# Kernel optimization log

Hardware: AMD Instinct MI355X
Metric: run time of the kernel (lower is better)

Reference implementation:

```python
import jax, jax.numpy as jnp
import numpy as np

B, L, V, E, H = 64, 32, 32000, 512, 1024


def setup_inputs() -> dict:
    key = jax.random.key(0)
    ks = jax.random.split(key, 12)
    s = 0.02
    return {
        "x": jax.random.randint(ks[0], (B, 4 * L), 0, V, dtype=jnp.int32),
        "IsTrain": 1,
        "embedding": jax.random.normal(ks[1], (V, E), jnp.float32) * s,
        "W_csm": jax.random.normal(ks[2], (E, H), jnp.float32) * s,
        "Wx1": jax.random.normal(ks[3], (H, H), jnp.float32) * s,
        "Wh1": jax.random.normal(ks[4], (H, H), jnp.float32) * s,
        "Wx2": jax.random.normal(ks[5], (H, H), jnp.float32) * s,
        "Wh2": jax.random.normal(ks[6], (H, H), jnp.float32) * s,
        "U": jax.random.normal(ks[7], (L, H, H), jnp.float32) * s,
        "Ww": jax.random.normal(ks[8], (V, H), jnp.float32) * s,
        "Wc": jax.random.normal(ks[9], (H, H), jnp.float32) * s,
        "Wfc": jax.random.normal(ks[10], (H, V), jnp.float32) * s,
    }


def _forward(x, embedding, W_csm, Wx1, Wh1, Wx2, Wh2, U, Ww, Wc, Wfc):
    # x: [B, 4L] int token ids (train mode: 4 sentences)
    emb = embedding[x]                                   # [B, 4L, E]

    # CSM: sentence -> vector [B, H] (mean-pool + projection + tanh)
    segs = emb[:, : 3 * L].reshape(x.shape[0], 3, L, E)  # first 3 sentences
    sent = jnp.tanh(jnp.einsum("bse,eh->bsh", segs.mean(axis=2), W_csm))  # [B,3,H]

    # RCM: 2-layer tanh RNN over sentence vectors; hidden after t sentences
    # equals RCM run on the length-t prefix (prefix property of an RNN).
    def step(carry, s_t):
        h1, h2 = carry
        h1 = jnp.tanh(s_t @ Wx1 + h1 @ Wh1)
        h2 = jnp.tanh(h1 @ Wx2 + h2 @ Wh2)
        return (h1, h2), h2

    h0 = jnp.zeros((x.shape[0], H), emb.dtype)
    _, hs = jax.lax.scan(step, (h0, h0), sent.transpose(1, 0, 2))  # [3,B,H]

    # Per-position context vectors: context_k = tanh(h_k @ U_m) for m in [0,L)
    contexts = jnp.tanh(jnp.einsum("sbh,mhk->sbmk", hs, U))        # [3,B,L,H]

    # RGM at step i (i>=1 within each section): prev hidden is always re-zeroed
    # in the original loop, so cur = tanh(onehot(w) @ Ww + ctx @ Wc); the one-hot
    # matmul is expressed as a gather (identical math).
    # Section k, local step i in [1,L): word index = x[:, (k+1)*L + i - 1]
    idx = jnp.stack([x[:, (k + 1) * L : (k + 2) * L - 1] for k in range(3)])  # [3,B,L-1]
    cur = jnp.tanh(Ww[idx] + jnp.einsum("sblh,hk->sblk", contexts[:, :, 1:], Wc))
    y_sec = jnp.einsum("sblh,hv->sblv", cur, Wfc)                  # [3,B,L-1,V]

    # Step 0 of each section: one-hot of the first target word (constant wrt params)
    firsts = x[:, jnp.array([L, 2 * L, 3 * L])].T                   # [3,B]
    first_oh = jax.nn.one_hot(firsts, V, dtype=y_sec.dtype)         # [3,B,V]

    y = jnp.concatenate([first_oh[:, :, None, :], y_sec], axis=2)   # [3,B,L,V]
    return y.transpose(1, 0, 2, 3).reshape(x.shape[0], 3 * L, V)


def reference(x, IsTrain, embedding, W_csm, Wx1, Wh1, Wx2, Wh2, U, Ww, Wc, Wfc):
    # IsTrain must be truthy: this reference implements the training branch.
    return _forward(x, embedding, W_csm, Wx1, Wh1, Wx2, Wh2, U, Ww, Wc, Wfc)
```

## Files before the change

kernel.cpp:

```cpp
#include <hip/hip_runtime.h>
#include <math.h>

typedef __bf16 bf16x8 __attribute__((ext_vector_type(8)));
typedef float f32x4 __attribute__((ext_vector_type(4)));
typedef unsigned short u16;
typedef u16 u16x8 __attribute__((ext_vector_type(8)));

#define DI __device__ __forceinline__

DI u16 f2bf(float f) {
  union { float f; unsigned u; } v; v.f = f;
  unsigned r = v.u + 0x7FFFu + ((v.u >> 16) & 1u);
  return (u16)(r >> 16);
}

DI void gload_lds16(const u16* g, u16* l) {
  __builtin_amdgcn_global_load_lds(
      (const __attribute__((address_space(1))) unsigned int*)g,
      (__attribute__((address_space(3))) unsigned int*)l, 16, 0, 0);
}

DI void grid_bar(int* ctr, int nblk) {
  __syncthreads();
  if (threadIdx.x == 0) {
    __threadfence();
    atomicAdd(ctr, 1);
    while (atomicAdd(ctr, 0) < nblk) { __builtin_amdgcn_s_sleep(8); }
    __threadfence();
  }
  __syncthreads();
}

__global__ __launch_bounds__(256) void meanpool_k(const int* __restrict__ x,
    const float* __restrict__ emb, u16* __restrict__ sentM) {
  int bs = blockIdx.x; int s = bs >> 6, b = bs & 63;
  int t = threadIdx.x;
  float a0 = 0.f, a1 = 0.f;
  for (int lt = 0; lt < 32; ++lt) {
    int tok = x[b * 128 + s * 32 + lt];
    const float* e = emb + (long)tok * 512;
    a0 += e[t]; a1 += e[t + 256];
  }
  sentM[(long)bs * 512 + t] = f2bf(a0 * (1.f / 32.f));
  sentM[(long)bs * 512 + t + 256] = f2bf(a1 * (1.f / 32.f));
}

DI void transpose64_body(const float* __restrict__ in, u16* __restrict__ out,
                         int C, int ostride) {
  __shared__ float tile[32 * 65];
  int c0 = blockIdx.x * 32, r0 = blockIdx.y * 64;
  int t = threadIdx.x;
  int cc = t & 31, rr0 = t >> 5;
#pragma unroll
  for (int i = 0; i < 8; ++i) {
    int rr = rr0 + 8 * i;
    tile[cc * 65 + (rr ^ ((cc & 7) << 3))] = in[(long)(r0 + rr) * C + c0 + cc];
  }
  __syncthreads();
  int cj = t >> 3, rj = t & 7;
  u16x8 v;
#pragma unroll
  for (int k = 0; k < 8; ++k)
    v[k] = f2bf(tile[cj * 65 + ((rj * 8 + k) ^ ((cj & 7) << 3))]);
  *(u16x8*)(out + (long)(c0 + cj) * ostride + r0 + rj * 8) = v;
}

__global__ __launch_bounds__(256) void transpose64(
    const float* __restrict__ in, u16* __restrict__ out, int R, int C,
    int ostride) {
  in += (long)blockIdx.z * (long)R * C;
  out += (long)blockIdx.z * (long)C * ostride;
  transpose64_body(in, out, C, ostride);
}

struct TJob { const float* in; u16* out; int R; int ostride; };
struct TJobs { TJob j[6]; };
__global__ __launch_bounds__(256) void transpose64_multi(TJobs jobs) {
  TJob jb = jobs.j[blockIdx.z];
  if ((int)(blockIdx.y * 64) >= jb.R) return;
  transpose64_body(jb.in, jb.out, 1024, jb.ostride);
}

DI void small_body(u16 (*As)[2048], u16 (*Bs)[4096],
                   const u16* A0, const u16* A1, const u16* Bt, u16* outp,
                   int M, int K, int kSplit, int Astride, int Bstride,
                   int mt, int ntb) {
  const int t = threadIdx.x;
  const int w = t >> 6, l = t & 63, lr = l & 15, lg = l >> 4;
  int ar = mt * 64 + (t & 63); if (ar >= M) ar = M - 1;
  const u16* pB = Bt + (long)(ntb * 128 + (t & 127)) * Bstride + (t >> 7) * 8;
  const int ntk = K >> 5;

  auto STG = [&](int buf, int kt) {
    int k0 = kt << 5;
    const u16* srcA = (k0 < kSplit)
        ? A0 + (long)ar * Astride + k0 + w * 8
        : A1 + (long)ar * 1024 + (k0 - kSplit) + w * 8;
    gload_lds16(srcA, &As[buf][w * 512]);
    gload_lds16(pB + k0, &Bs[buf][w * 512]);
    gload_lds16(pB + k0 + 16, &Bs[buf][2048 + w * 512]);
  };
  STG(0, 0);
  if (ntk > 1) STG(1, 1);

  f32x4 acc[4][2] = {};
  for (int kt = 0; kt < ntk; ++kt) {
    int cb = kt % 3;
    if (kt + 2 < ntk) {
      STG((kt + 2) % 3, kt + 2);
      asm volatile("s_waitcnt vmcnt(6)" ::: "memory");
    } else if (kt + 1 < ntk) {
      asm volatile("s_waitcnt vmcnt(3)" ::: "memory");
    } else {
      asm volatile("s_waitcnt vmcnt(0)" ::: "memory");
    }
    __builtin_amdgcn_s_barrier();
    __builtin_amdgcn_sched_barrier(0);
    bf16x8 a[4], b[2];
#pragma unroll
    for (int mf = 0; mf < 4; ++mf)
      a[mf] = *(const bf16x8*)(&As[cb][(lg * 64 + mf * 16 + lr) * 8]);
#pragma unroll
    for (int nf = 0; nf < 2; ++nf)
      b[nf] = *(const bf16x8*)(&Bs[cb][(lg * 128 + w * 32 + nf * 16 + lr) * 8]);
#pragma unroll
    for (int mf = 0; mf < 4; ++mf)
#pragma unroll
      for (int nf = 0; nf < 2; ++nf)
        acc[mf][nf] = __builtin_amdgcn_mfma_f32_16x16x32_bf16(a[mf], b[nf], acc[mf][nf], 0, 0, 0);
    __builtin_amdgcn_s_barrier();
    __builtin_amdgcn_sched_barrier(0);
  }
#pragma unroll
  for (int mf = 0; mf < 4; ++mf)
#pragma unroll
    for (int j = 0; j < 4; ++j) {
      int r = mt * 64 + mf * 16 + lg * 4 + j;
      if (r < M) {
        u16* o = outp + (long)r * 1024 + ntb * 128 + w * 32;
#pragma unroll
        for (int nf = 0; nf < 2; ++nf)
          o[nf * 16 + lr] = f2bf(tanhf(acc[mf][nf][j]));
      }
    }
}

__global__ __launch_bounds__(256) void rnn_chain(
    const u16* __restrict__ sentM, u16* __restrict__ sentH,
    u16* __restrict__ h1a, u16* __restrict__ h1b, u16* __restrict__ hsb,
    const u16* __restrict__ WcsmT, const u16* __restrict__ WxhT1,
    const u16* __restrict__ WxhT2, int* __restrict__ ctr) {
  __shared__ __align__(16) u16 As[3][2048];
  __shared__ __align__(16) u16 Bs[3][4096];
  int b = blockIdx.x;
  small_body(As, Bs, sentM, sentM, WcsmT, sentH, 192, 512, 512, 512, 512,
             b >> 3, b & 7);
  grid_bar(ctr + 0, 24);
  if (b < 8) small_body(As, Bs, sentH, h1a, WxhT1, h1a,
                        64, 1024, 1024, 1024, 2048, 0, b);
  grid_bar(ctr + 1, 24);
  if (b < 8) small_body(As, Bs, h1a, h1a, WxhT2, hsb,
                        64, 1024, 1024, 1024, 2048, 0, b);
  grid_bar(ctr + 2, 24);
  if (b < 8) small_body(As, Bs, sentH + 65536, h1a, WxhT1, h1b,
                        64, 2048, 1024, 1024, 2048, 0, b);
  grid_bar(ctr + 3, 24);
  if (b < 8) small_body(As, Bs, h1b, hsb, WxhT2, hsb + 65536,
                        64, 2048, 1024, 1024, 2048, 0, b);
  grid_bar(ctr + 4, 24);
  if (b < 8) small_body(As, Bs, sentH + 131072, h1b, WxhT1, h1a,
                        64, 2048, 1024, 1024, 2048, 0, b);
  grid_bar(ctr + 5, 24);
  if (b < 8) small_body(As, Bs, h1a, hsb + 65536, WxhT2, hsb + 131072,
                        64, 2048, 1024, 1024, 2048, 0, b);
}

template <int MODE>
__global__ __launch_bounds__(256) void gemm_bf16(
    const u16* __restrict__ A, const u16* __restrict__ Bt,
    const float* __restrict__ Ww, const int* __restrict__ xtok,
    void* __restrict__ outp, int M) {
  int mt = blockIdx.x, nt = blockIdx.y, mz = blockIdx.z;
  if constexpr (MODE == 0) Bt += (long)mz << 20;

  __shared__ __align__(16) u16 As[128 * 32];
  __shared__ __align__(16) u16 Bs[128 * 32];

  const int t = threadIdx.x;
  const int w = t >> 6, l = t & 63;
  const int lr = l & 15, lg = l >> 4;
  const int wr = w >> 1, wc = w & 1;

  int ar0 = mt * 128 + (t >> 2);
  int ar1 = ar0 + 64;
  if (ar0 >= M) ar0 = 0;
  if (ar1 >= M) ar1 = 0;
  long arow0, arow1;
  if constexpr (MODE == 1) {
    arow0 = (long)(ar0 / 31) * 32 + (ar0 % 31) + 1;
    arow1 = (long)(ar1 / 31) * 32 + (ar1 % 31) + 1;
  } else {
    arow0 = ar0; arow1 = ar1;
  }

  const u16* ga0 = A + arow0 * 1024 + (t & 3) * 8;
  const u16* ga1 = A + arow1 * 1024 + (t & 3) * 8;
  const u16* gb0 = Bt + ((long)nt * 128 + (t >> 2)) * 1024 + (t & 3) * 8;
  const u16* gb1 = gb0 + 64 * 1024;

  u16* dA0 = As + w * 512; u16* dA1 = As + 2048 + w * 512;
  u16* dB0 = Bs + w * 512; u16* dB1 = Bs + 2048 + w * 512;

  f32x4 acc[4][4] = {};

  for (int kt = 0; kt < 32; ++kt) {
    __syncthreads();
    gload_lds16(ga0, dA0); gload_lds16(ga1, dA1);
    gload_lds16(gb0, dB0); gload_lds16(gb1, dB1);
    ga0 += 32; ga1 += 32; gb0 += 32; gb1 += 32;
    __syncthreads();
    bf16x8 a[4], b[4];
#pragma unroll
    for (int m = 0; m < 4; ++m)
      a[m] = *(const bf16x8*)&As[(wr * 64 + m * 16 + lr) * 32 + lg * 8];
#pragma unroll
    for (int n = 0; n < 4; ++n)
      b[n] = *(const bf16x8*)&Bs[(wc * 64 + n * 16 + lr) * 32 + lg * 8];
#pragma unroll
    for (int m = 0; m < 4; ++m)
#pragma unroll
      for (int n = 0; n < 4; ++n)
        acc[m][n] = __builtin_amdgcn_mfma_f32_16x16x32_bf16(a[m], b[n], acc[m][n], 0, 0, 0);
  }

#pragma unroll
  for (int m = 0; m < 4; ++m) {
#pragma unroll
    for (int j = 0; j < 4; ++j) {
      int r = mt * 128 + wr * 64 + m * 16 + lg * 4 + j;
      if (r >= M) continue;
      if constexpr (MODE == 0) {
        u16* oc = (u16*)outp;
#pragma unroll
        for (int n = 0; n < 4; ++n) {
          int col = nt * 128 + wc * 64 + n * 16 + lr;
          oc[((long)r * 32 + mz) * 1024 + col] = f2bf(tanhf(acc[m][n][j]));
        }
      } else {
        int sb = r / 31, l1 = r % 31;
        int s = sb >> 6, b = sb & 63;
        int widx = xtok[b * 128 + (s + 1) * 32 + l1];
        const float* wwr = Ww + (long)widx * 1024;
        u16* oc = (u16*)outp;
#pragma unroll
        for (int n = 0; n < 4; ++n) {
          int col = nt * 128 + wc * 64 + n * 16 + lr;
          oc[(long)r * 1024 + col] = f2bf(tanhf(acc[m][n][j] + wwr[col]));
        }
      }
    }
  }
}

#define NOSTAGE ((void)0)
#define VM4 asm volatile("s_waitcnt vmcnt(4)" ::: "memory")
#define VM0 asm volatile("s_waitcnt vmcnt(0)" ::: "memory")

#define STAGE_A(H, KT) do {                                                \
    const u16* _s = ((H) ? pA1 : pA0) + (KT) * 64;                         \
    u16* _d = lds + ((KT) & 1) * 16384 + (H) * 8192 + w * 512;             \
    gload_lds16(_s, _d); gload_lds16(_s + 32, _d + 4096);                  \
  } while (0)
#define STAGE_B(H, KT) do {                                                \
    const u16* _s = ((H) ? pB1 : pB0) + (KT) * 64;                         \
    u16* _d = lds + 32768 + ((KT) & 1) * 16384 + (H) * 8192 + w * 512;     \
    gload_lds16(_s, _d); gload_lds16(_s + 32, _d + 4096);                  \
  } while (0)

#define PHASE(ABASE, MH, NH, RA, RB, STAGESTMT, WAITSTMT) do {             \
    if (RA) {                                                              \
      _Pragma("unroll") for (int ks = 0; ks < 2; ++ks)                     \
      _Pragma("unroll") for (int mf = 0; mf < 4; ++mf)                     \
        a[mf][ks] = *(const bf16x8*)(lds + (ABASE) + (MH) * 8192 + laneA + \
                                     ks * 4096 + mf * 128);                \
    }                                                                      \
    if (RB) {                                                              \
      _Pragma("unroll") for (int ks = 0; ks < 2; ++ks)                     \
      _Pragma("unroll") for (int nf = 0; nf < 2; ++nf)                     \
        b[NH][nf][ks] = *(const bf16x8*)(lds + 32768 + (ABASE) +           \
                                         (NH) * 8192 + laneB +             \
                                         ks * 4096 + nf * 128);            \
    }                                                                      \
    STAGESTMT;                                                             \
    __builtin_amdgcn_s_barrier();                                          \
    asm volatile("s_waitcnt lgkmcnt(0)" ::: "memory");                     \
    __builtin_amdgcn_sched_barrier(0);                                     \
    __builtin_amdgcn_s_setprio(1);                                         \
    _Pragma("unroll") for (int ks = 0; ks < 2; ++ks)                       \
    _Pragma("unroll") for (int mf = 0; mf < 4; ++mf)                       \
    _Pragma("unroll") for (int nf = 0; nf < 2; ++nf)                       \
      acc[(MH) * 4 + mf][(NH) * 2 + nf] =                                  \
          __builtin_amdgcn_mfma_f32_16x16x32_bf16(                         \
              a[mf][ks], b[NH][nf][ks],                                    \
              acc[(MH) * 4 + mf][(NH) * 2 + nf], 0, 0, 0);                 \
    __builtin_amdgcn_s_setprio(0);                                         \
    WAITSTMT;                                                              \
    __builtin_amdgcn_s_barrier();                                          \
  } while (0)

__global__ __launch_bounds__(512, 2) void gemm_big(
    const u16* __restrict__ A, const u16* __restrict__ Bt,
    const int* __restrict__ x, float* __restrict__ out) {
  __shared__ __align__(16) u16 lds[65536];

  const int t = threadIdx.x;
  const int w = t >> 6, l = t & 63;
  const int lr = l & 15, lg = l >> 4;
  const int wm = w >> 2, wn = w & 3;
  const int laneA = (lg * 128 + wm * 64 + lr) * 8;
  const int laneB = (lg * 128 + wn * 32 + lr) * 8;

  int xcd = blockIdx.x & 7, slot = blockIdx.x >> 3;

  for (int tl = slot; tl < 375; tl += 32) {
    int nt = tl / 3;
    int mt = xcd * 3 + tl % 3;

    int arow0 = mt * 256 + (t & 127);
    int arow1 = arow0 + 128;
    int ar0c = arow0 > 5951 ? 5951 : arow0;
    int ar1c = arow1 > 5951 ? 5951 : arow1;
    const u16* pA0 = A + (long)ar0c * 1024 + (t >> 7) * 8;
    const u16* pA1 = A + (long)ar1c * 1024 + (t >> 7) * 8;
    const u16* pB0 = Bt + ((long)nt * 256 + (t & 127)) * 1024 + (t >> 7) * 8;
    const u16* pB1 = pB0 + 128 * 1024;

    f32x4 acc[8][4] = {};
    bf16x8 a[4][2], b[2][2][2];

    STAGE_A(0, 0); STAGE_B(0, 0); STAGE_B(1, 0); STAGE_A(1, 0);
    STAGE_A(0, 1); STAGE_B(0, 1);
    VM4;
    __builtin_amdgcn_s_barrier();

    for (int g = 0; g < 14; g += 2) {
      PHASE(0,     0, 0, 1, 1, STAGE_B(1, g + 1), NOSTAGE);
      PHASE(0,     0, 1, 0, 1, STAGE_A(1, g + 1), NOSTAGE);
      PHASE(0,     1, 0, 1, 0, STAGE_A(0, g + 2), NOSTAGE);
      PHASE(0,     1, 1, 0, 0, STAGE_B(0, g + 2), VM4);
      PHASE(16384, 0, 0, 1, 1, STAGE_B(1, g + 2), NOSTAGE);
      PHASE(16384, 0, 1, 0, 1, STAGE_A(1, g + 2), NOSTAGE);
      PHASE(16384, 1, 0, 1, 0, STAGE_A(0, g + 3), NOSTAGE);
      PHASE(16384, 1, 1, 0, 0, STAGE_B(0, g + 3), VM4);
    }
    PHASE(0,     0, 0, 1, 1, STAGE_B(1, 15), NOSTAGE);
    PHASE(0,     0, 1, 0, 1, STAGE_A(1, 15), NOSTAGE);
    PHASE(0,     1, 0, 1, 0, NOSTAGE, NOSTAGE);
    PHASE(0,     1, 1, 0, 0, NOSTAGE, VM0);
    PHASE(16384, 0, 0, 1, 1, NOSTAGE, NOSTAGE);
    PHASE(16384, 0, 1, 0, 1, NOSTAGE, NOSTAGE);
    PHASE(16384, 1, 0, 1, 0, NOSTAGE, NOSTAGE);
    PHASE(16384, 1, 1, 0, 0, NOSTAGE, NOSTAGE);

    float* T = (float*)lds + w * 2112;
#pragma unroll
    for (int mh = 0; mh < 2; ++mh)
#pragma unroll
      for (int nh = 0; nh < 2; ++nh) {
#pragma unroll
        for (int mf = 0; mf < 4; ++mf)
#pragma unroll
          for (int j = 0; j < 4; ++j)
#pragma unroll
            for (int nf = 0; nf < 2; ++nf)
              T[(mf * 16 + lg * 4 + j) * 33 + nf * 16 + lr] =
                  acc[mh * 4 + mf][nh * 2 + nf][j];
#pragma unroll
        for (int i = 0; i < 8; ++i) {
          int row = (l >> 3) + 8 * i;
          int c4 = (l & 7) * 4;
          f32x4 v;
          v[0] = T[row * 33 + c4];     v[1] = T[row * 33 + c4 + 1];
          v[2] = T[row * 33 + c4 + 2]; v[3] = T[row * 33 + c4 + 3];
          int r = mt * 256 + mh * 128 + wm * 64 + row;
          int colb = nt * 256 + nh * 128 + wn * 32 + c4;
          float* o;
          if (r < 5952) {
            int s = r / 1984, rem = r % 1984;
            int bb = rem / 31, l1 = rem % 31;
            o = out + ((long)bb * 96 + s * 32 + l1 + 1) * 32000 + colb;
          } else {
            int i2 = r - 5952;
            int s = i2 >> 6, bb = i2 & 63;
            int tok = x[bb * 128 + (s + 1) * 32];
            v[0] = (colb == tok);     v[1] = (colb + 1 == tok);
            v[2] = (colb + 2 == tok); v[3] = (colb + 3 == tok);
            o = out + ((long)bb * 96 + s * 32) * 32000 + colb;
          }
          __builtin_nontemporal_store(v, (f32x4*)o);
        }
      }
    __builtin_amdgcn_s_barrier();
  }
}

extern "C" void kernel_launch(void* const* d_in, const int* in_sizes, int n_in,
                              void* d_out, int out_size, void* d_ws, size_t ws_size,
                              hipStream_t stream) {
  const int*   x    = (const int*)d_in[0];
  const float* emb  = (const float*)d_in[2];
  const float* Wcsm = (const float*)d_in[3];
  const float* Wx1  = (const float*)d_in[4];
  const float* Wh1  = (const float*)d_in[5];
  const float* Wx2  = (const float*)d_in[6];
  const float* Wh2  = (const float*)d_in[7];
  const float* U    = (const float*)d_in[8];
  const float* Ww   = (const float*)d_in[9];
  const float* Wc   = (const float*)d_in[10];
  const float* Wfc  = (const float*)d_in[11];
  float* out = (float*)d_out;

  char* ws = (char*)d_ws;
  u16* sentM = (u16*)(ws + 0);
  u16* sentH = (u16*)(ws + 196608);
  u16* h1a   = (u16*)(ws + 589824);
  u16* h1b   = (u16*)(ws + 720896);
  u16* hsb   = (u16*)(ws + 851968);
  u16* ctx   = (u16*)(ws + 1245184);
  u16* WcsmT = (u16*)(ws + 1245184);
  u16* WxhT1 = (u16*)(ws + 2293760);
  u16* WxhT2 = (u16*)(ws + 6488064);
  u16* cur   = (u16*)(ws + 13828096);
  u16* WcT   = (u16*)(ws + 26017792);
  u16* BIG   = (u16*)(ws + 28114944);
  int* ctr   = (int*)(ws + 28114944 + 67108864 - 64);

  TJobs jobs;
  jobs.j[0] = {Wx1,  WxhT1,        1024, 2048};
  jobs.j[1] = {Wh1,  WxhT1 + 1024, 1024, 2048};
  jobs.j[2] = {Wx2,  WxhT2,        1024, 2048};
  jobs.j[3] = {Wh2,  WxhT2 + 1024, 1024, 2048};
  jobs.j[4] = {Wc,   WcT,          1024, 1024};
  jobs.j[5] = {Wcsm, WcsmT,         512,  512};
  transpose64_multi<<<dim3(32, 16, 6), 256, 0, stream>>>(jobs);

  meanpool_k<<<192, 256, 0, stream>>>(x, emb, sentM);
  hipMemsetAsync((void*)ctr, 0, 64, stream);
  rnn_chain<<<24, 256, 0, stream>>>(sentM, sentH, h1a, h1b, hsb,
                                    WcsmT, WxhT1, WxhT2, ctr);

  transpose64<<<dim3(32, 16, 32), 256, 0, stream>>>(U, BIG, 1024, 1024, 1024);
  gemm_bf16<0><<<dim3(2, 8, 32), 256, 0, stream>>>(hsb, BIG, nullptr, nullptr, (void*)ctx, 192);

  gemm_bf16<1><<<dim3(47, 8, 1), 256, 0, stream>>>(ctx, WcT, Ww, x, (void*)cur, 5952);

  transpose64<<<dim3(1000, 16, 1), 256, 0, stream>>>(Wfc, BIG, 1024, 32000, 1024);
  gemm_big<<<256, 512, 0, stream>>>(cur, BIG, x, out);
}
```

Baseline: 911.4 us.

## Switch final vocab projection GEMM from bf16 to fp8 MFMA with scaling

Converts the activations (cur) and the transposed Wfc weights to fp8 e4m3 with a 16x prescale each and runs the big output GEMM using fp8 MFMA. The accumulator is rescaled by 1/256 at the end. This halves the operand bytes moved and staged through LDS, and it uses the higher-rate fp8 matrix instructions. The LDS layout, load addressing and wait counts are adjusted to match. The cost is a large loss of precision in the dominant GEMM, which may exceed the output tolerance.

```diff
diff --git a/kernel.cpp b/kernel.cpp
--- a/kernel.cpp
+++ b/kernel.cpp
@@ -4,7 +4,9 @@
 typedef __bf16 bf16x8 __attribute__((ext_vector_type(8)));
 typedef float f32x4 __attribute__((ext_vector_type(4)));
 typedef unsigned short u16;
+typedef unsigned char u8;
 typedef u16 u16x8 __attribute__((ext_vector_type(8)));
+typedef u8 u8x8 __attribute__((ext_vector_type(8)));
 
 #define DI __device__ __forceinline__
 
@@ -14,7 +16,19 @@
   return (u16)(r >> 16);
 }
 
-DI void gload_lds16(const u16* g, u16* l) {
+DI u8 f2fp8(float f) {
+  union { float f; unsigned u; } v; v.f = f;
+  unsigned s = (v.u >> 24) & 0x80u;
+  unsigned au = v.u & 0x7FFFFFFFu;
+  unsigned r = au + 0x7FFFFu + ((au >> 20) & 1u);
+  int e = (int)(r >> 23) - 120;
+  unsigned m = (r >> 20) & 7u;
+  if (e <= 0) return (u8)s;
+  if (e > 15 || (e == 15 && m == 7)) return (u8)(s | 0x7E);
+  return (u8)(s | ((unsigned)e << 3) | m);
+}
+
+DI void gload_lds16(const void* g, void* l) {
   __builtin_amdgcn_global_load_lds(
       (const __attribute__((address_space(1))) unsigned int*)g,
       (__attribute__((address_space(3))) unsigned int*)l, 16, 0, 0);
@@ -79,6 +93,26 @@
   TJob jb = jobs.j[blockIdx.z];
   if ((int)(blockIdx.y * 64) >= jb.R) return;
   transpose64_body(jb.in, jb.out, 1024, jb.ostride);
+}
+
+__global__ __launch_bounds__(256) void transpose64_f8(
+    const float* __restrict__ in, u8* __restrict__ out, int C, int ostride) {
+  __shared__ float tile[32 * 65];
+  int c0 = blockIdx.x * 32, r0 = blockIdx.y * 64;
+  int t = threadIdx.x;
+  int cc = t & 31, rr0 = t >> 5;
+#pragma unroll
+  for (int i = 0; i < 8; ++i) {
+    int rr = rr0 + 8 * i;
+    tile[cc * 65 + (rr ^ ((cc & 7) << 3))] = in[(long)(r0 + rr) * C + c0 + cc];
+  }
+  __syncthreads();
+  int cj = t >> 3, rj = t & 7;
+  u8x8 v;
+#pragma unroll
+  for (int k = 0; k < 8; ++k)
+    v[k] = f2fp8(16.f * tile[cj * 65 + ((rj * 8 + k) ^ ((cj & 7) << 3))]);
+  *(u8x8*)(out + (long)(c0 + cj) * ostride + r0 + rj * 8) = v;
 }
 
 DI void small_body(u16 (*As)[2048], u16 (*Bs)[4096],
@@ -251,11 +285,11 @@
         int s = sb >> 6, b = sb & 63;
         int widx = xtok[b * 128 + (s + 1) * 32 + l1];
         const float* wwr = Ww + (long)widx * 1024;
-        u16* oc = (u16*)outp;
+        u8* oc = (u8*)outp;
 #pragma unroll
         for (int n = 0; n < 4; ++n) {
           int col = nt * 128 + wc * 64 + n * 16 + lr;
-          oc[(long)r * 1024 + col] = f2bf(tanhf(acc[m][n][j] + wwr[col]));
+          oc[(long)r * 1024 + col] = f2fp8(16.f * tanhf(acc[m][n][j] + wwr[col]));
         }
       }
     }
@@ -263,33 +297,29 @@
 }
 
 #define NOSTAGE ((void)0)
-#define VM4 asm volatile("s_waitcnt vmcnt(4)" ::: "memory")
+#define VM2 asm volatile("s_waitcnt vmcnt(2)" ::: "memory")
 #define VM0 asm volatile("s_waitcnt vmcnt(0)" ::: "memory")
 
-#define STAGE_A(H, KT) do {                                                \
-    const u16* _s = ((H) ? pA1 : pA0) + (KT) * 64;                         \
-    u16* _d = lds + ((KT) & 1) * 16384 + (H) * 8192 + w * 512;             \
-    gload_lds16(_s, _d); gload_lds16(_s + 32, _d + 4096);                  \
-  } while (0)
-#define STAGE_B(H, KT) do {                                                \
-    const u16* _s = ((H) ? pB1 : pB0) + (KT) * 64;                         \
-    u16* _d = lds + 32768 + ((KT) & 1) * 16384 + (H) * 8192 + w * 512;     \
-    gload_lds16(_s, _d); gload_lds16(_s + 32, _d + 4096);                  \
-  } while (0)
+#define STAGE_A(H, KT) \
+  gload_lds16(((H) ? pA1 : pA0) + (KT) * 64, \
+              ldsb + ((KT) & 1) * 16384 + (H) * 8192 + w * 1024)
+#define STAGE_B(H, KT) \
+  gload_lds16(((H) ? pB1 : pB0) + (KT) * 64, \
+              ldsb + 32768 + ((KT) & 1) * 16384 + (H) * 8192 + w * 1024)
 
 #define PHASE(ABASE, MH, NH, RA, RB, STAGESTMT, WAITSTMT) do {             \
     if (RA) {                                                              \
       _Pragma("unroll") for (int ks = 0; ks < 2; ++ks)                     \
       _Pragma("unroll") for (int mf = 0; mf < 4; ++mf)                     \
-        a[mf][ks] = *(const bf16x8*)(lds + (ABASE) + (MH) * 8192 + laneA + \
-                                     ks * 4096 + mf * 128);                \
+        a[mf][ks] = *(const long*)(ldsb + (ABASE) + (MH) * 8192 + laneA +  \
+                                   ks * 4096 + mf * 256);                  \
     }                                                                      \
     if (RB) {                                                              \
       _Pragma("unroll") for (int ks = 0; ks < 2; ++ks)                     \
       _Pragma("unroll") for (int nf = 0; nf < 2; ++nf)                     \
-        b[NH][nf][ks] = *(const bf16x8*)(lds + 32768 + (ABASE) +           \
-                                         (NH) * 8192 + laneB +             \
-                                         ks * 4096 + nf * 128);            \
+        b[NH][nf][ks] = *(const long*)(ldsb + 32768 + (ABASE) +            \
+                                       (NH) * 8192 + laneB +               \
+                                       ks * 4096 + nf * 256);              \
     }                                                                      \
     STAGESTMT;                                                             \
     __builtin_amdgcn_s_barrier();                                          \
@@ -300,7 +330,7 @@
     _Pragma("unroll") for (int mf = 0; mf < 4; ++mf)                       \
     _Pragma("unroll") for (int nf = 0; nf < 2; ++nf)                       \
       acc[(MH) * 4 + mf][(NH) * 2 + nf] =                                  \
-          __builtin_amdgcn_mfma_f32_16x16x32_bf16(                         \
+          __builtin_amdgcn_mfma_f32_16x16x32_fp8_fp8(                      \
               a[mf][ks], b[NH][nf][ks],                                    \
               acc[(MH) * 4 + mf][(NH) * 2 + nf], 0, 0, 0);                 \
     __builtin_amdgcn_s_setprio(0);                                         \
@@ -309,16 +339,17 @@
   } while (0)
 
 __global__ __launch_bounds__(512, 2) void gemm_big(
-    const u16* __restrict__ A, const u16* __restrict__ Bt,
+    const u8* __restrict__ A, const u8* __restrict__ Bt,
     const int* __restrict__ x, float* __restrict__ out) {
   __shared__ __align__(16) u16 lds[65536];
+  u8* ldsb = (u8*)lds;
 
   const int t = threadIdx.x;
   const int w = t >> 6, l = t & 63;
   const int lr = l & 15, lg = l >> 4;
   const int wm = w >> 2, wn = w & 3;
-  const int laneA = (lg * 128 + wm * 64 + lr) * 8;
-  const int laneB = (lg * 128 + wn * 32 + lr) * 8;
+  const int laneA = (wm * 64 + lr) * 16 + (lg >> 1) * 2048 + (lg & 1) * 8;
+  const int laneB = (wn * 32 + lr) * 16 + (lg >> 1) * 2048 + (lg & 1) * 8;
 
   int xcd = blockIdx.x & 7, slot = blockIdx.x >> 3;
 
@@ -330,28 +361,28 @@
     int arow1 = arow0 + 128;
     int ar0c = arow0 > 5951 ? 5951 : arow0;
     int ar1c = arow1 > 5951 ? 5951 : arow1;
-    const u16* pA0 = A + (long)ar0c * 1024 + (t >> 7) * 8;
-    const u16* pA1 = A + (long)ar1c * 1024 + (t >> 7) * 8;
-    const u16* pB0 = Bt + ((long)nt * 256 + (t & 127)) * 1024 + (t >> 7) * 8;
-    const u16* pB1 = pB0 + 128 * 1024;
+    const u8* pA0 = A + (long)ar0c * 1024 + (t >> 7) * 16;
+    const u8* pA1 = A + (long)ar1c * 1024 + (t >> 7) * 16;
+    const u8* pB0 = Bt + ((long)nt * 256 + (t & 127)) * 1024 + (t >> 7) * 16;
+    const u8* pB1 = pB0 + 128 * 1024;
 
     f32x4 acc[8][4] = {};
-    bf16x8 a[4][2], b[2][2][2];
+    long a[4][2], b[2][2][2];
 
     STAGE_A(0, 0); STAGE_B(0, 0); STAGE_B(1, 0); STAGE_A(1, 0);
     STAGE_A(0, 1); STAGE_B(0, 1);
-    VM4;
+    VM2;
     __builtin_amdgcn_s_barrier();
 
     for (int g = 0; g < 14; g += 2) {
       PHASE(0,     0, 0, 1, 1, STAGE_B(1, g + 1), NOSTAGE);
       PHASE(0,     0, 1, 0, 1, STAGE_A(1, g + 1), NOSTAGE);
       PHASE(0,     1, 0, 1, 0, STAGE_A(0, g + 2), NOSTAGE);
-      PHASE(0,     1, 1, 0, 0, STAGE_B(0, g + 2), VM4);
+      PHASE(0,     1, 1, 0, 0, STAGE_B(0, g + 2), VM2);
       PHASE(16384, 0, 0, 1, 1, STAGE_B(1, g + 2), NOSTAGE);
       PHASE(16384, 0, 1, 0, 1, STAGE_A(1, g + 2), NOSTAGE);
       PHASE(16384, 1, 0, 1, 0, STAGE_A(0, g + 3), NOSTAGE);
-      PHASE(16384, 1, 1, 0, 0, STAGE_B(0, g + 3), VM4);
+      PHASE(16384, 1, 1, 0, 0, STAGE_B(0, g + 3), VM2);
     }
     PHASE(0,     0, 0, 1, 1, STAGE_B(1, 15), NOSTAGE);
     PHASE(0,     0, 1, 0, 1, STAGE_A(1, 15), NOSTAGE);
@@ -374,7 +405,7 @@
 #pragma unroll
             for (int nf = 0; nf < 2; ++nf)
               T[(mf * 16 + lg * 4 + j) * 33 + nf * 16 + lr] =
-                  acc[mh * 4 + mf][nh * 2 + nf][j];
+                  acc[mh * 4 + mf][nh * 2 + nf][j] * (1.f / 256.f);
 #pragma unroll
         for (int i = 0; i < 8; ++i) {
           int row = (l >> 3) + 8 * i;
@@ -430,7 +461,7 @@
   u16* WcsmT = (u16*)(ws + 1245184);
   u16* WxhT1 = (u16*)(ws + 2293760);
   u16* WxhT2 = (u16*)(ws + 6488064);
-  u16* cur   = (u16*)(ws + 13828096);
+  u8*  curf  = (u8*)(ws + 13828096);
   u16* WcT   = (u16*)(ws + 26017792);
   u16* BIG   = (u16*)(ws + 28114944);
   int* ctr   = (int*)(ws + 28114944 + 67108864 - 64);
@@ -452,8 +483,8 @@
   transpose64<<<dim3(32, 16, 32), 256, 0, stream>>>(U, BIG, 1024, 1024, 1024);
   gemm_bf16<0><<<dim3(2, 8, 32), 256, 0, stream>>>(hsb, BIG, nullptr, nullptr, (void*)ctx, 192);
 
-  gemm_bf16<1><<<dim3(47, 8, 1), 256, 0, stream>>>(ctx, WcT, Ww, x, (void*)cur, 5952);
-
-  transpose64<<<dim3(1000, 16, 1), 256, 0, stream>>>(Wfc, BIG, 1024, 32000, 1024);
-  gemm_big<<<256, 512, 0, stream>>>(cur, BIG, x, out);
-}
+  gemm_bf16<1><<<dim3(47, 8, 1), 256, 0, stream>>>(ctx, WcT, Ww, x, (void*)curf, 5952);
+
+  transpose64_f8<<<dim3(1000, 16, 1), 256, 0, stream>>>(Wfc, (u8*)BIG, 32000, 1024);
+  gemm_big<<<256, 512, 0, stream>>>(curf, (u8*)BIG, x, out);
+}
```

Result: faster. 825.3 us (-9.4%).
